# Performance work log

Hardware: AMD Instinct MI355X
Metric: run time of the kernel (lower is better)

The kernel has to match this reference:

```python
import jax, jax.numpy as jnp
import numpy as np

EPS = 1e-12
W_MAX = 0.8
ALPHA_MAX = 1.5
T = 10
ETA = 0.2
ALPHA_SCALE = 1.0
N = 50000
IN_DIM = 512
HID = 256
C = 8
EH = 64
E2 = 400000  # undirected pairs; E = 2*E2 directed edges


def setup_inputs() -> dict:
    key = jax.random.key(0)
    ks = jax.random.split(key, 12)
    x = jax.random.normal(ks[0], (N, IN_DIM), jnp.float32)
    src0 = jax.random.randint(ks[1], (E2,), 0, N)
    dst0 = jax.random.randint(ks[2], (E2,), 0, N)
    edge_index = jnp.concatenate([jnp.stack([src0, dst0]), jnp.stack([dst0, src0])], axis=1)
    rev = jnp.concatenate([jnp.arange(E2) + E2, jnp.arange(E2)])
    def lin(k, i, o):
        return jax.random.normal(k, (i, o), jnp.float32) * (2.0 / i) ** 0.5
    enc_w1 = lin(ks[3], IN_DIM, HID); enc_b1 = jnp.zeros((HID,), jnp.float32)
    enc_w2 = lin(ks[4], HID, C); enc_b2 = jnp.zeros((C,), jnp.float32)
    edge_w1 = lin(ks[5], 2 * HID + 2, EH); edge_b1 = jnp.zeros((EH,), jnp.float32)
    edge_w2 = lin(ks[6], EH, 1); edge_b2 = jnp.zeros((1,), jnp.float32)
    bound = (6.0 / (C + C)) ** 0.5  # xavier_uniform
    R_raw = jax.random.uniform(ks[7], (C, C), jnp.float32, -bound, bound) + 0.5 * jnp.eye(C, dtype=jnp.float32)
    R_scale_log = jnp.float32(0.0)
    msg_logit = jnp.float32(-3.0)
    return dict(x=x, edge_index=edge_index, rev=rev,
                enc_w1=enc_w1, enc_b1=enc_b1, enc_w2=enc_w2, enc_b2=enc_b2,
                edge_w1=edge_w1, edge_b1=edge_b1, edge_w2=edge_w2, edge_b2=edge_b2,
                R_raw=R_raw, R_scale_log=R_scale_log, msg_logit=msg_logit)


def reference(x, edge_index, rev, enc_w1, enc_b1, enc_w2, enc_b2,
              edge_w1, edge_b1, edge_w2, edge_b2, R_raw, R_scale_log, msg_logit):
    num_nodes = x.shape[0]
    src, dst = edge_index[0], edge_index[1]
    # unary encoder (mlp type, eval mode -> no dropout)
    h = jax.nn.relu(x @ enc_w1 + enc_b1)
    logits = h @ enc_w2 + enc_b2
    log_phi = jax.nn.log_softmax(logits, axis=-1)  # [N, C]
    # structural edge features from out-degree of src
    deg = jax.ops.segment_sum(jnp.ones_like(src, jnp.float32), src, num_segments=num_nodes)
    logdeg = jnp.log(deg + 1.0)
    a, b = logdeg[src], logdeg[dst]
    struct = jnp.stack([a + b, jnp.abs(a - b)], axis=-1)  # [E, 2]
    # learned symmetric edge weights -> per-edge kernel K
    hs, hd = h[src], h[dst]
    edge_in = jnp.concatenate([hs * hd, jnp.abs(hs - hd), struct], axis=-1)  # [E, 2H+2]
    eh = jax.nn.relu(edge_in @ edge_w1 + edge_b1)
    w_raw = (eh @ edge_w2 + edge_b2)[:, 0]
    w = W_MAX * jax.nn.sigmoid(w_raw)
    w = 0.5 * (w + w[rev])
    R = 0.5 * (R_raw + R_raw.T)
    R = (jax.nn.softplus(R_scale_log) + 1e-06) * jnp.tanh(R)
    K = jnp.exp(w[:, None, None] * R[None])  # [E, C, C]
    degc = jnp.maximum(deg, 1.0)
    edge_norm = (degc[src] * degc[dst]) ** -0.5  # [E]
    alpha = ALPHA_MAX * jax.nn.sigmoid(msg_logit) * ALPHA_SCALE
    lp_src = log_phi[src]
    m = jax.nn.softmax(lp_src, axis=-1)  # init_unary=True

    def step(m, _):
        f = jnp.einsum('ec,ecd->ed', m, K)
        log_f = jnp.log(jnp.maximum(f, EPS)) * edge_norm[:, None]
        sum_in = jax.ops.segment_sum(log_f, dst, num_segments=num_nodes)
        excl = sum_in[src] - log_f[rev]
        m_new = jax.nn.softmax(lp_src + alpha * excl, axis=-1)
        m = (1.0 - ETA) * m + ETA * m_new
        m = jnp.maximum(m, EPS)
        m = m / m.sum(axis=-1, keepdims=True)
        return m, None

    m, _ = jax.lax.scan(step, m, None, length=T)
    # beliefs
    f = jnp.einsum('ec,ecd->ed', m, K)
    log_f = jnp.log(jnp.maximum(f, EPS)) * edge_norm[:, None]
    sum_in = jax.ops.segment_sum(log_f, dst, num_segments=num_nodes)
    beliefs = jax.nn.softmax(log_phi + alpha * sum_in, axis=-1)
    return beliefs
```

## Files before the change

### kernel.cpp

```cpp
#include <hip/hip_runtime.h>
#include <cstddef>
#include <cstdint>

typedef _Float16 h4 __attribute__((ext_vector_type(4)));
typedef _Float16 h8 __attribute__((ext_vector_type(8)));
typedef float    f4 __attribute__((ext_vector_type(4)));
typedef int      i4 __attribute__((ext_vector_type(4)));

#define NN      50000
#define IND     512
#define HIDN    256
#define E2P     400000
#define EDD     800000
#define NBLK    196
#define SCN     50176
#define EBLK    1563
#define NBPN    1563

#define OFF_HF16    ((size_t)0)
#define OFF_LOGFA   ((size_t)0)
#define OFF_LOGFB   ((size_t)12800000)
#define OFF_Z       ((size_t)25600000)
#define OFF_DEG     ((size_t)28800000)
#define OFF_LOGDEG  ((size_t)29004800)
#define OFF_DEGC    ((size_t)29204800)
#define OFF_BASE    ((size_t)29404800)
#define OFF_CNT     ((size_t)29609600)
#define OFF_BLK     ((size_t)29814400)
#define OFF_WT      ((size_t)29818496)
#define OFF_BT      ((size_t)30080640)
#define OFF_RS      ((size_t)30150272)
#define OFF_WSYM    ((size_t)30150784)
#define OFF_POS     ((size_t)31750784)
#define OFF_ORDER   ((size_t)34950784)
#define OFF_BASE2   ((size_t)36550784)
#define OFF_OFS2    ((size_t)36755584)
#define OFF_EIS     ((size_t)36960384)
#define OFF_M       ((size_t)40160384)
#define OFF_WNS     ((size_t)52960384)
#define OFF_PPOS    ((size_t)59360384)
#define WS_NEED     ((size_t)62560384)

__device__ __forceinline__ int key2(int s, int d) {
    return ((s >> 10) << 10) | (d >> 6);
}

__device__ __forceinline__ int xcd_swz(int bid, int nwg) {
    int q = nwg >> 3, r = nwg & 7;
    int x = bid & 7, idx = bid >> 3;
    return (x < r ? x * (q + 1) : r * (q + 1) + (x - r) * q) + idx;
}

__global__ void k_deg(const int* __restrict__ ei, int* __restrict__ deg,
                      int* __restrict__ cnt2) {
    int e = blockIdx.x * 256 + threadIdx.x;
    int v = ei[e];
    atomicAdd(&deg[v], 1);
    if (e < E2P) {
        int d = ei[EDD + e];
        atomicAdd(&cnt2[key2(v, d)], 1);
    }
}

__global__ void k_node(const int* __restrict__ deg, float* __restrict__ logdeg,
                       float* __restrict__ degc) {
    int n = blockIdx.x * 256 + threadIdx.x;
    if (n < NN) {
        float d = (float)deg[n];
        logdeg[n] = logf(d + 1.0f);
        degc[n]   = fmaxf(d, 1.0f);
    }
}

__global__ void k_scan1(const int* __restrict__ deg, int* __restrict__ incl,
                        int* __restrict__ blk) {
    __shared__ int sm[256];
    int i = blockIdx.x * 256 + threadIdx.x;
    int v = deg[i];
    sm[threadIdx.x] = v;
    __syncthreads();
    for (int off = 1; off < 256; off <<= 1) {
        int t = (threadIdx.x >= off) ? sm[threadIdx.x - off] : 0;
        __syncthreads();
        sm[threadIdx.x] += t;
        __syncthreads();
    }
    incl[i] = sm[threadIdx.x];
    if (threadIdx.x == 255) blk[blockIdx.x] = sm[255];
}

__global__ void k_scan2(int* __restrict__ blk) {
    __shared__ int sm[256];
    int v = (threadIdx.x < NBLK) ? blk[threadIdx.x] : 0;
    sm[threadIdx.x] = v;
    __syncthreads();
    for (int off = 1; off < 256; off <<= 1) {
        int t = (threadIdx.x >= off) ? sm[threadIdx.x - off] : 0;
        __syncthreads();
        sm[threadIdx.x] += t;
        __syncthreads();
    }
    if (threadIdx.x < NBLK) blk[threadIdx.x] = sm[threadIdx.x];
}

__global__ void k_scan3(const int* __restrict__ incl, const int* __restrict__ deg,
                        const int* __restrict__ blk, int* __restrict__ base) {
    int i = blockIdx.x * 256 + threadIdx.x;
    int off = (blockIdx.x > 0) ? blk[blockIdx.x - 1] : 0;
    base[i] = off + incl[i] - deg[i];
}

__global__ void k_pos(const int* __restrict__ ei, const int* __restrict__ base,
                      int* __restrict__ cnt, int* __restrict__ pos) {
    int e = blockIdx.x * 256 + threadIdx.x;
    int dstn = ei[EDD + e];
    pos[e] = base[dstn] + atomicAdd(&cnt[dstn], 1);
}

__global__ void k_order(const int* __restrict__ ei, const int* __restrict__ base2,
                        int* __restrict__ ofs2, int* __restrict__ order) {
    int p = blockIdx.x * 256 + threadIdx.x;
    if (p < E2P) {
        int k = key2(ei[p], ei[EDD + p]);
        order[base2[k] + atomicAdd(&ofs2[k], 1)] = p;
    }
}

__global__ void k_gath(const int* __restrict__ ei, const int* __restrict__ order,
                       int2* __restrict__ eiS) {
    int i = blockIdx.x * 256 + threadIdx.x;
    if (i < E2P) {
        int p = order[i];
        eiS[i] = make_int2(ei[p], ei[EDD + p]);
    }
}

__global__ void k_prep(const float* __restrict__ enc_w1, const float* __restrict__ edge_w1,
                       const float* __restrict__ R_raw, const float* __restrict__ Rsl,
                       const float* __restrict__ mlog,
                       _Float16* __restrict__ Wt, _Float16* __restrict__ Bt,
                       float* __restrict__ Rs) {
    int gid = blockIdx.x * 256 + threadIdx.x;
    if (gid < 256 * 512) {
        int n = gid >> 9, k = gid & 511;
        Wt[n * 512 + k] = (_Float16)enc_w1[k * 256 + n];
        return;
    }
    int g2 = gid - 256 * 512;
    if (g2 < 64 * 544) {
        int n = g2 / 544, k = g2 - n * 544;
        float v = 0.0f;
        if (k < 512) {
            int tm = k >> 5, r = k & 31;
            int qq = r >> 3, jj = (r >> 1) & 3, typ = k & 1;
            int c = (tm >> 1) * 32 + qq * 8 + (tm & 1) * 4 + jj;
            v = edge_w1[(typ ? 256 + c : c) * 64 + n];
        } else if (k < 514) {
            v = edge_w1[k * 64 + n];
        }
        Bt[n * 544 + k] = (_Float16)v;
        return;
    }
    int g3 = g2 - 64 * 544;
    if (g3 < 64) {
        int c = g3 >> 3, d = g3 & 7;
        float rv = 0.5f * (R_raw[c * 8 + d] + R_raw[d * 8 + c]);
        float s  = log1pf(expf(Rsl[0])) + 1e-6f;
        Rs[g3] = s * tanhf(rv);
        return;
    }
    if (g3 == 64) {
        Rs[64] = 1.5f / (1.0f + expf(-mlog[0]));
    }
}

__global__ __launch_bounds__(256) void k_enc(const float* __restrict__ x,
                                             const _Float16* __restrict__ Wt,
                                             const float* __restrict__ b1,
                                             _Float16* __restrict__ hf) {
    __shared__ _Float16 WL[2][256 * 40];
    const int tid = threadIdx.x;
    const int wid = tid >> 6;
    const int lane = tid & 63;
    const int l15 = lane & 15;
    const int q = lane >> 4;
    const int m0 = blockIdx.x * 64;
    const int row = m0 + wid * 16 + l15;
    const bool ract = (row < NN);
    const float* xrow = x + (size_t)row * IND;

    f4 acc[16];
#pragma unroll
    for (int i = 0; i < 16; i++) acc[i] = (f4){0.f, 0.f, 0.f, 0.f};

    const int wn  = tid >> 2;
    const int wo  = (tid & 3) * 8;

    h8 wreg[4];
#pragma unroll
    for (int rep = 0; rep < 4; rep++)
        wreg[rep] = *(const h8*)(Wt + (size_t)(rep * 64 + wn) * IND + wo);
    f4 xa = (f4){0, 0, 0, 0}, xb = (f4){0, 0, 0, 0};
    if (ract) {
        const f4* xp = (const f4*)(xrow + q * 8);
        xa = xp[0]; xb = xp[1];
    }

    for (int kt = 0; kt < 16; kt++) {
        const int cur = kt & 1;
#pragma unroll
        for (int rep = 0; rep < 4; rep++)
            *(h8*)&WL[cur][(rep * 64 + wn) * 40 + wo] = wreg[rep];
        __syncthreads();
        f4 xa2, xb2;
        if (kt < 15) {
            const int kc = (kt + 1) * 32;
#pragma unroll
            for (int rep = 0; rep < 4; rep++)
                wreg[rep] = *(const h8*)(Wt + (size_t)(rep * 64 + wn) * IND + kc + wo);
            if (ract) {
                const f4* xp = (const f4*)(xrow + kc + q * 8);
                xa2 = xp[0]; xb2 = xp[1];
            }
        }
        h8 a;
#pragma unroll
        for (int u = 0; u < 4; u++) { a[u] = (_Float16)xa[u]; a[4 + u] = (_Float16)xb[u]; }
#pragma unroll
        for (int nt = 0; nt < 16; nt++) {
            h8 b = *(const h8*)&WL[cur][(nt * 16 + l15) * 40 + q * 8];
            acc[nt] = __builtin_amdgcn_mfma_f32_16x16x32_f16(a, b, acc[nt], 0, 0, 0);
        }
        if (kt < 15 && ract) { xa = xa2; xb = xb2; }
        __syncthreads();
    }
#pragma unroll
    for (int nt = 0; nt < 16; nt++) {
        int col = nt * 16 + l15;
        float bv = b1[col];
#pragma unroll
        for (int reg = 0; reg < 4; reg++) {
            int orow = m0 + wid * 16 + q * 4 + reg;
            if (orow < NN) {
                float v = acc[nt][reg] + bv;
                hf[(size_t)orow * HIDN + col] = (_Float16)fmaxf(v, 0.f);
            }
        }
    }
}

__global__ void k_logits(const _Float16* __restrict__ hf, const float* __restrict__ w2,
                         const float* __restrict__ b2, float* __restrict__ Z) {
    __shared__ float w2L[2048];
    for (int i = threadIdx.x; i < 2048; i += 256) w2L[i] = w2[i];
    __syncthreads();
    int n = blockIdx.x * 256 + threadIdx.x;
    if (n >= NN) return;
    float sum[8];
#pragma unroll
    for (int c = 0; c < 8; c++) sum[c] = b2[c];
    for (int kb = 0; kb < 32; kb++) {
        h8 hv = *(const h8*)(hf + (size_t)n * HIDN + kb * 8);
#pragma unroll
        for (int u = 0; u < 8; u++) {
            float hx = (float)hv[u];
            const float* wr = &w2L[(kb * 8 + u) * 8];
#pragma unroll
            for (int c = 0; c < 8; c++) sum[c] += hx * wr[c];
        }
    }
    float mx = sum[0];
#pragma unroll
    for (int c = 1; c < 8; c++) mx = fmaxf(mx, sum[c]);
    float se = 0.f;
#pragma unroll
    for (int c = 0; c < 8; c++) se += __expf(sum[c] - mx);
    float lse = __logf(se);
#pragma unroll
    for (int c = 0; c < 8; c++) Z[(size_t)n * 16 + c] = sum[c] - mx - lse;
}

__global__ __launch_bounds__(256) void k_edge(const int2* __restrict__ eiS,
        const _Float16* __restrict__ hf, const float* __restrict__ logdeg,
        const _Float16* __restrict__ BtG, const float* __restrict__ eb1,
        const float* __restrict__ ew2, const float* __restrict__ eb2,
        float* __restrict__ wsym2) {
    __shared__ _Float16 BtL[64 * 136];
    const int tid = threadIdx.x;
    const int wid = tid >> 6;
    const int lane = tid & 63;
    const int l15 = lane & 15;
    const int q = lane >> 4;
    const int eb = xcd_swz(blockIdx.x, gridDim.x) * 128;

    int sidx[2], didx[2];
    float la[2], lb[2];
#pragma unroll
    for (int mt = 0; mt < 2; mt++) {
        int e = eb + wid * 32 + mt * 16 + l15;
        int2 sd = eiS[e];
        sidx[mt] = sd.x;
        didx[mt] = sd.y;
        la[mt] = logdeg[sidx[mt]];
        lb[mt] = logdeg[didx[mt]];
    }

    f4 acc[2][4];
#pragma unroll
    for (int a = 0; a < 2; a++)
#pragma unroll
        for (int b = 0; b < 4; b++) acc[a][b] = (f4){0.f, 0.f, 0.f, 0.f};

    const _Float16* hq = hf + q * 8;
    h8 curS[2], curD[2];
#pragma unroll
    for (int mt = 0; mt < 2; mt++) {
        curS[mt] = *(const h8*)(hq + (size_t)sidx[mt] * HIDN);
        curD[mt] = *(const h8*)(hq + (size_t)didx[mt] * HIDN);
    }

    for (int ph = 0; ph < 4; ph++) {
        __syncthreads();
        {
            const int r = tid >> 2;
            const int c0 = tid & 3;
            const int kbase = ph * 128;
#pragma unroll
            for (int i2 = 0; i2 < 4; i2++) {
                int ck = c0 + i2 * 4;
                *(h8*)&BtL[r * 136 + ck * 8] =
                    *(const h8*)(BtG + (size_t)r * 544 + kbase + ck * 8);
            }
        }
        __syncthreads();
#pragma unroll
        for (int kk2 = 0; kk2 < 2; kk2++) {
            const int kk = ph * 2 + kk2;
            h8 nxtS[2], nxtD[2];
            if (kk < 7) {
                const int c1 = (kk + 1) * 32;
#pragma unroll
                for (int mt = 0; mt < 2; mt++) {
                    nxtS[mt] = *(const h8*)(hq + (size_t)sidx[mt] * HIDN + c1);
                    nxtD[mt] = *(const h8*)(hq + (size_t)didx[mt] * HIDN + c1);
                }
            }
            const int ko = kk2 * 64 + q * 8;
            {
                h8 a0[2];
#pragma unroll
                for (int mt = 0; mt < 2; mt++) {
#pragma unroll
                    for (int j = 0; j < 4; j++) {
                        float x1 = (float)curS[mt][j], x2 = (float)curD[mt][j];
                        a0[mt][2 * j]     = (_Float16)(x1 * x2);
                        a0[mt][2 * j + 1] = (_Float16)fabsf(x1 - x2);
                    }
                }
                h8 bf[4];
#pragma unroll
                for (int nt = 0; nt < 4; nt++)
                    bf[nt] = *(const h8*)&BtL[(nt * 16 + l15) * 136 + ko];
#pragma unroll
                for (int mt = 0; mt < 2; mt++)
#pragma unroll
                    for (int nt = 0; nt < 4; nt++)
                        acc[mt][nt] = __builtin_amdgcn_mfma_f32_16x16x32_f16(a0[mt], bf[nt], acc[mt][nt], 0, 0, 0);
            }
            {
                h8 a1[2];
#pragma unroll
                for (int mt = 0; mt < 2; mt++) {
#pragma unroll
                    for (int j = 0; j < 4; j++) {
                        float x1 = (float)curS[mt][4 + j], x2 = (float)curD[mt][4 + j];
                        a1[mt][2 * j]     = (_Float16)(x1 * x2);
                        a1[mt][2 * j + 1] = (_Float16)fabsf(x1 - x2);
                    }
                }
                h8 bf[4];
#pragma unroll
                for (int nt = 0; nt < 4; nt++)
                    bf[nt] = *(const h8*)&BtL[(nt * 16 + l15) * 136 + ko + 32];
#pragma unroll
                for (int mt = 0; mt < 2; mt++)
#pragma unroll
                    for (int nt = 0; nt < 4; nt++)
                        acc[mt][nt] = __builtin_amdgcn_mfma_f32_16x16x32_f16(a1[mt], bf[nt], acc[mt][nt], 0, 0, 0);
            }
            if (kk < 7) {
#pragma unroll
                for (int mt = 0; mt < 2; mt++) { curS[mt] = nxtS[mt]; curD[mt] = nxtD[mt]; }
            }
        }
    }

    __syncthreads();
    {
        const int r = tid >> 2, ck = tid & 3;
        *(h8*)&BtL[r * 136 + ck * 8] = *(const h8*)(BtG + (size_t)r * 544 + 512 + ck * 8);
    }
    __syncthreads();
    {
        h8 bf[4];
#pragma unroll
        for (int nt = 0; nt < 4; nt++)
            bf[nt] = *(const h8*)&BtL[(nt * 16 + l15) * 136 + q * 8];
#pragma unroll
        for (int mt = 0; mt < 2; mt++) {
            h8 a = (h8){0, 0, 0, 0, 0, 0, 0, 0};
            if (q == 0) {
                a[0] = (_Float16)(la[mt] + lb[mt]);
                a[1] = (_Float16)fabsf(la[mt] - lb[mt]);
            }
#pragma unroll
            for (int nt = 0; nt < 4; nt++)
                acc[mt][nt] = __builtin_amdgcn_mfma_f32_16x16x32_f16(a, bf[nt], acc[mt][nt], 0, 0, 0);
        }
    }

    float b1v[4], w2v[4];
#pragma unroll
    for (int nt = 0; nt < 4; nt++) {
        int col = nt * 16 + l15;
        b1v[nt] = eb1[col];
        w2v[nt] = ew2[col];
    }
    const float b2s = eb2[0];
    float part[2][4];
#pragma unroll
    for (int mt = 0; mt < 2; mt++)
#pragma unroll
        for (int reg = 0; reg < 4; reg++) {
            float s = 0.f;
#pragma unroll
            for (int nt = 0; nt < 4; nt++) {
                float v = acc[mt][nt][reg] + b1v[nt];
                s += fmaxf(v, 0.f) * w2v[nt];
            }
            part[mt][reg] = s;
        }
#pragma unroll
    for (int off = 1; off < 16; off <<= 1)
#pragma unroll
        for (int mt = 0; mt < 2; mt++)
#pragma unroll
            for (int reg = 0; reg < 4; reg++)
                part[mt][reg] += __shfl_xor(part[mt][reg], off, 64);
    if (l15 == 0) {
#pragma unroll
        for (int mt = 0; mt < 2; mt++)
#pragma unroll
            for (int reg = 0; reg < 4; reg++) {
                int er = eb + wid * 32 + mt * 16 + q * 4 + reg;
                if (er < E2P) {
                    float xr = part[mt][reg] + b2s;
                    wsym2[er] = 0.8f / (1.0f + __expf(-xr));
                }
            }
    }
}


__device__ __forceinline__ void kprod1(const float* __restrict__ RsL, float w,
                                       const float* m, float* f) {
#pragma unroll
    for (int d = 0; d < 8; d++) f[d] = 0.f;
#pragma unroll
    for (int c = 0; c < 8; c++) {
        {
            float kv = __expf(w * RsL[c * 8 + c]);
            f[c] += m[c] * kv;
        }
#pragma unroll
        for (int d = c + 1; d < 8; d++) {
            float kv = __expf(w * RsL[c * 8 + d]);
            f[d] += m[c] * kv;
            f[c] += m[d] * kv;
        }
    }
}

__global__ __launch_bounds__(256) void k_init(const int2* __restrict__ eiS,
        const float* __restrict__ wsym2, const float* __restrict__ degc,
        const float* __restrict__ Rs, const float* __restrict__ Z,
        const int* __restrict__ pos, const int* __restrict__ order,
        float2* __restrict__ wnS, int* __restrict__ ppos,
        _Float16* __restrict__ M, _Float16* __restrict__ logfA) {
    __shared__ float RsL[64];
    const int tid = threadIdx.x;
    if (tid < 64) RsL[tid] = Rs[tid];
    __syncthreads();
    int i = xcd_swz(blockIdx.x, EBLK) * 256 + tid;
    if (i >= E2P) return;
    int p = order[i];
    int2 sd = eiS[i];
    int sp = sd.x, dp = sd.y;
    float w = wsym2[i];
    float nrm = rsqrtf(degc[sp] * degc[dp]);
    int pz0 = pos[p];
    int pz1 = pos[E2P + p];
    wnS[pz0] = make_float2(w, nrm);
    wnS[pz1] = make_float2(w, nrm);
    ppos[pz0] = pz1;
    ppos[pz1] = pz0;
    const f4* Zs = (const f4*)(Z + (size_t)sp * 16);
    const f4* Zd = (const f4*)(Z + (size_t)dp * 16);
    f4 ls0 = Zs[0], ls1 = Zs[1], ld0 = Zd[0], ld1 = Zd[1];
    float lps[8], lpd[8];
#pragma unroll
    for (int u = 0; u < 4; u++) { lps[u] = ls0[u]; lps[4+u] = ls1[u]; lpd[u] = ld0[u]; lpd[4+u] = ld1[u]; }
    float me[8], mr[8];
    {
        float mx = lps[0], mx2 = lpd[0];
#pragma unroll
        for (int d = 1; d < 8; d++) { mx = fmaxf(mx, lps[d]); mx2 = fmaxf(mx2, lpd[d]); }
        float s = 0.f, s2 = 0.f;
#pragma unroll
        for (int d = 0; d < 8; d++) { me[d] = __expf(lps[d] - mx); s += me[d];
                                      mr[d] = __expf(lpd[d] - mx2); s2 += mr[d]; }
        float rs = 1.f / s, rs2 = 1.f / s2;
#pragma unroll
        for (int d = 0; d < 8; d++) { me[d] *= rs; mr[d] *= rs2; }
    }
    {
        h8 mh, mh2;
#pragma unroll
        for (int d = 0; d < 8; d++) { mh[d] = (_Float16)me[d]; mh2[d] = (_Float16)mr[d]; }
        *(h8*)(M + (size_t)pz1 * 8) = mh;
        *(h8*)(M + (size_t)pz0 * 8) = mh2;
    }
    float fe[8], fr[8];
    kprod1(RsL, w, me, fe);
    kprod1(RsL, w, mr, fr);
    h8 le, lr;
#pragma unroll
    for (int d = 0; d < 8; d++) {
        le[d] = (_Float16)(__logf(fmaxf(fe[d], 1e-12f)) * nrm);
        lr[d] = (_Float16)(__logf(fmaxf(fr[d], 1e-12f)) * nrm);
    }
    *(h8*)(logfA + (size_t)pz0 * 8) = le;
    *(h8*)(logfA + (size_t)pz1 * 8) = lr;
}

__global__ __launch_bounds__(256) void k_bpN(const float* __restrict__ Rs,
        const float* __restrict__ Z, const int* __restrict__ base,
        const int* __restrict__ deg, const float2* __restrict__ wnS,
        const int* __restrict__ ppos, _Float16* __restrict__ M,
        const _Float16* __restrict__ lfA, _Float16* __restrict__ lfB) {
    __shared__ float RsL[64];
    const int tid = threadIdx.x;
    if (tid < 64) RsL[tid] = Rs[tid];
    __syncthreads();
    int g = xcd_swz(blockIdx.x, NBPN) * 256 + tid;
    int n = g >> 3;
    if (n >= NN) return;
    const int j = tid & 7;
    const int b = base[n], cnt = deg[n];
    const float alpha = Rs[64];
    const f4* Zr = (const f4*)(Z + (size_t)n * 16);
    f4 z0 = Zr[0], z1 = Zr[1];
    float lp[8];
#pragma unroll
    for (int u = 0; u < 4; u++) { lp[u] = z0[u]; lp[4 + u] = z1[u]; }
    float S[8];
#pragma unroll
    for (int d = 0; d < 8; d++) S[d] = 0.f;
    for (int s = j; s < cnt; s += 8) {
        h8 v = *(const h8*)(lfA + (size_t)(b + s) * 8);
#pragma unroll
        for (int d = 0; d < 8; d++) S[d] += (float)v[d];
    }
#pragma unroll
    for (int off = 1; off < 8; off <<= 1)
#pragma unroll
        for (int d = 0; d < 8; d++) S[d] += __shfl_xor(S[d], off, 64);
    for (int s = j; s < cnt; s += 8) {
        const int sl = b + s;
        h8 lfh = *(const h8*)(lfA + (size_t)sl * 8);
        h8 mh  = *(const h8*)(M + (size_t)sl * 8);
        float2 wn = wnS[sl];
        float t[8], m1[8];
#pragma unroll
        for (int d = 0; d < 8; d++)
            t[d] = lp[d] + alpha * (S[d] - (float)lfh[d]);
        float mx = t[0];
#pragma unroll
        for (int d = 1; d < 8; d++) mx = fmaxf(mx, t[d]);
        float ssum = 0.f;
#pragma unroll
        for (int d = 0; d < 8; d++) { m1[d] = __expf(t[d] - mx); ssum += m1[d]; }
        float rs = 1.f / ssum, t1 = 0.f;
#pragma unroll
        for (int d = 0; d < 8; d++) {
            m1[d] = fmaxf(0.8f * (float)mh[d] + 0.2f * m1[d] * rs, 1e-12f);
            t1 += m1[d];
        }
        float rt = 1.f / t1;
#pragma unroll
        for (int d = 0; d < 8; d++) m1[d] *= rt;
        h8 mo;
#pragma unroll
        for (int d = 0; d < 8; d++) mo[d] = (_Float16)m1[d];
        *(h8*)(M + (size_t)sl * 8) = mo;
        float f2[8];
        kprod1(RsL, wn.x, m1, f2);
        h8 le;
#pragma unroll
        for (int d = 0; d < 8; d++)
            le[d] = (_Float16)(__logf(fmaxf(f2[d], 1e-12f)) * wn.y);
        *(h8*)(lfB + (size_t)ppos[sl] * 8) = le;
    }
}

__global__ void k_sum(const _Float16* __restrict__ logf, const int* __restrict__ base,
                      const int* __restrict__ deg, const float* __restrict__ Z,
                      const float* __restrict__ Rs, float* __restrict__ out) {
    int g = blockIdx.x * 256 + threadIdx.x;
    int n = g >> 3;
    if (n >= NN) return;
    int j = threadIdx.x & 7;
    int b = base[n], cnt = deg[n];
    float acc[8];
#pragma unroll
    for (int d = 0; d < 8; d++) acc[d] = 0.f;
    for (int s = j; s < cnt; s += 8) {
        h8 v = *(const h8*)(logf + (size_t)(b + s) * 8);
#pragma unroll
        for (int d = 0; d < 8; d++) acc[d] += (float)v[d];
    }
    int lane = threadIdx.x & 63;
    float v4[4], v2[2], r;
    {
        bool hi = (lane & 4) != 0;
#pragma unroll
        for (int i = 0; i < 4; i++) {
            float send = hi ? acc[i] : acc[i + 4];
            float recv = __shfl_xor(send, 4, 64);
            v4[i] = (hi ? acc[i + 4] : acc[i]) + recv;
        }
    }
    {
        bool hi = (lane & 2) != 0;
#pragma unroll
        for (int i = 0; i < 2; i++) {
            float send = hi ? v4[i] : v4[i + 2];
            float recv = __shfl_xor(send, 2, 64);
            v2[i] = (hi ? v4[i + 2] : v4[i]) + recv;
        }
    }
    {
        bool hi = (lane & 1) != 0;
        float send = hi ? v2[0] : v2[1];
        float recv = __shfl_xor(send, 1, 64);
        r = (hi ? v2[1] : v2[0]) + recv;
    }
    float alpha = Rs[64];
    float v = Z[(size_t)n * 16 + j] + alpha * r;
    float mx = v;
    mx = fmaxf(mx, __shfl_xor(mx, 1, 64));
    mx = fmaxf(mx, __shfl_xor(mx, 2, 64));
    mx = fmaxf(mx, __shfl_xor(mx, 4, 64));
    float ex = __expf(v - mx);
    float s = ex;
    s += __shfl_xor(s, 1, 64); s += __shfl_xor(s, 2, 64); s += __shfl_xor(s, 4, 64);
    out[(size_t)n * 8 + j] = ex / s;
}

extern "C" void kernel_launch(void* const* d_in, const int* in_sizes, int n_in,
                              void* d_out, int out_size, void* d_ws, size_t ws_size,
                              hipStream_t stream) {
    if (ws_size < WS_NEED) return;
    const float* x        = (const float*)d_in[0];
    const int*   ei       = (const int*)d_in[1];
    const float* enc_w1   = (const float*)d_in[3];
    const float* enc_b1   = (const float*)d_in[4];
    const float* enc_w2   = (const float*)d_in[5];
    const float* enc_b2   = (const float*)d_in[6];
    const float* edge_w1  = (const float*)d_in[7];
    const float* edge_b1  = (const float*)d_in[8];
    const float* edge_w2  = (const float*)d_in[9];
    const float* edge_b2  = (const float*)d_in[10];
    const float* R_raw    = (const float*)d_in[11];
    const float* Rsl      = (const float*)d_in[12];
    const float* mlog     = (const float*)d_in[13];

    char* ws = (char*)d_ws;
    _Float16* hf     = (_Float16*)(ws + OFF_HF16);
    _Float16* lfA    = (_Float16*)(ws + OFF_LOGFA);
    _Float16* lfB    = (_Float16*)(ws + OFF_LOGFB);
    float* Zb        = (float*)(ws + OFF_Z);
    int*   deg       = (int*)  (ws + OFF_DEG);
    float* logdeg    = (float*)(ws + OFF_LOGDEG);
    float* degc      = (float*)(ws + OFF_DEGC);
    int*   baseA     = (int*)  (ws + OFF_BASE);
    int*   cnt       = (int*)  (ws + OFF_CNT);
    int*   blk       = (int*)  (ws + OFF_BLK);
    _Float16* Wt     = (_Float16*)(ws + OFF_WT);
    _Float16* Bt     = (_Float16*)(ws + OFF_BT);
    float* Rs        = (float*)(ws + OFF_RS);
    float* wsym2     = (float*)(ws + OFF_WSYM);
    int*   pos       = (int*)  (ws + OFF_POS);
    int*   order     = (int*)  (ws + OFF_ORDER);
    int*   base2     = (int*)  (ws + OFF_BASE2);
    int*   ofs2      = (int*)  (ws + OFF_OFS2);
    int2*  eiS       = (int2*) (ws + OFF_EIS);
    _Float16* Mb     = (_Float16*)(ws + OFF_M);
    float2* wnS      = (float2*)(ws + OFF_WNS);
    int*   ppos      = (int*)  (ws + OFF_PPOS);
    float* outp      = (float*)d_out;

    hipMemsetAsync(deg, 0, (size_t)SCN * 4, stream);
    hipMemsetAsync(ofs2, 0, (size_t)SCN * 4, stream);
    k_deg<<<dim3(EDD / 256), dim3(256), 0, stream>>>(ei, deg, ofs2);
    k_node<<<dim3(NBLK), dim3(256), 0, stream>>>(deg, logdeg, degc);
    k_prep<<<dim3((256 * 512 + 64 * 544 + 65 + 255) / 256), dim3(256), 0, stream>>>(
        enc_w1, edge_w1, R_raw, Rsl, mlog, Wt, Bt, Rs);
    k_scan1<<<dim3(NBLK), dim3(256), 0, stream>>>(deg, cnt , blk);
    k_scan2<<<dim3(1), dim3(256), 0, stream>>>(blk);
    k_scan3<<<dim3(NBLK), dim3(256), 0, stream>>>(cnt, deg, blk, baseA);
    hipMemsetAsync(cnt, 0, (size_t)SCN * 4, stream);
    k_pos<<<dim3(EDD / 256), dim3(256), 0, stream>>>(ei, baseA, cnt, pos);
    k_scan1<<<dim3(NBLK), dim3(256), 0, stream>>>(ofs2, cnt, blk);
    k_scan2<<<dim3(1), dim3(256), 0, stream>>>(blk);
    k_scan3<<<dim3(NBLK), dim3(256), 0, stream>>>(cnt, ofs2, blk, base2);
    hipMemsetAsync(ofs2, 0, (size_t)SCN * 4, stream);
    k_order<<<dim3(EBLK), dim3(256), 0, stream>>>(ei, base2, ofs2, order);
    k_gath<<<dim3(EBLK), dim3(256), 0, stream>>>(ei, order, eiS);
    k_enc<<<dim3((NN + 63) / 64), dim3(256), 0, stream>>>(x, Wt, enc_b1, hf);
    k_logits<<<dim3(NBLK), dim3(256), 0, stream>>>(hf, enc_w2, enc_b2, Zb);
    k_edge<<<dim3(E2P / 128), dim3(256), 0, stream>>>(eiS, hf, logdeg, Bt, edge_b1,
                                                      edge_w2, edge_b2, wsym2);
    k_init<<<dim3(EBLK), dim3(256), 0, stream>>>(eiS, wsym2, degc, Rs, Zb, pos, order,
                                                 wnS, ppos, Mb, lfA);
    _Float16* cur = lfA;
    _Float16* nxt = lfB;
    for (int t = 0; t < 10; t++) {
        k_bpN<<<dim3(NBPN), dim3(256), 0, stream>>>(Rs, Zb, baseA, deg, wnS, ppos,
                                                    Mb, cur, nxt);
        _Float16* tmp = cur; cur = nxt; nxt = tmp;
    }
    k_sum<<<dim3((NN * 8 + 255) / 256), dim3(256), 0, stream>>>(cur, baseA, deg, Zb,
                                                                Rs, outp);
    (void)in_sizes; (void)n_in; (void)out_size;
}
```

Measured before the change: 805.0 us.

## Switch BP log-message storage to source-ordered layout with LDS-staged block gather

The BP step now writes log-messages contiguously at the edge's own slot and gathers incoming ones through ppos. Each block handles 32 nodes and stages their gathered log-messages in LDS, so the segment sums and the per-edge updates reuse them instead of rereading global memory. Scattered writes become coalesced writes, and the random access moves to the read side. The encoder GEMM also preloads the whole x row strip into registers and fully unrolls its K loop, which raises register pressure (launch bounds set to one block).

```diff
diff --git a/kernel.cpp b/kernel.cpp
--- a/kernel.cpp
+++ b/kernel.cpp
@@ -16,6 +16,7 @@
 #define SCN     50176
 #define EBLK    1563
 #define NBPN    1563
+#define BCAP    1024
 
 #define OFF_HF16    ((size_t)0)
 #define OFF_LOGFA   ((size_t)0)
@@ -174,10 +175,10 @@
     }
 }
 
-__global__ __launch_bounds__(256) void k_enc(const float* __restrict__ x,
-                                             const _Float16* __restrict__ Wt,
-                                             const float* __restrict__ b1,
-                                             _Float16* __restrict__ hf) {
+__global__ __launch_bounds__(256, 1) void k_enc(const float* __restrict__ x,
+                                                const _Float16* __restrict__ Wt,
+                                                const float* __restrict__ b1,
+                                                _Float16* __restrict__ hf) {
     __shared__ _Float16 WL[2][256 * 40];
     const int tid = threadIdx.x;
     const int wid = tid >> 6;
@@ -189,49 +190,56 @@
     const bool ract = (row < NN);
     const float* xrow = x + (size_t)row * IND;
 
+    f4 xk0[16], xk1[16];
+#pragma unroll
+    for (int kt = 0; kt < 16; kt++) {
+        if (ract) {
+            const f4* xp = (const f4*)(xrow + kt * 32 + q * 8);
+            xk0[kt] = xp[0]; xk1[kt] = xp[1];
+        } else {
+            xk0[kt] = (f4){0, 0, 0, 0}; xk1[kt] = (f4){0, 0, 0, 0};
+        }
+    }
+    h8 xh[16];
+#pragma unroll
+    for (int kt = 0; kt < 16; kt++) {
+#pragma unroll
+        for (int u = 0; u < 4; u++) {
+            xh[kt][u]     = (_Float16)xk0[kt][u];
+            xh[kt][4 + u] = (_Float16)xk1[kt][u];
+        }
+    }
+
     f4 acc[16];
 #pragma unroll
     for (int i = 0; i < 16; i++) acc[i] = (f4){0.f, 0.f, 0.f, 0.f};
 
-    const int wn  = tid >> 2;
-    const int wo  = (tid & 3) * 8;
+    const int wn = tid >> 2;
+    const int wo = (tid & 3) * 8;
 
     h8 wreg[4];
 #pragma unroll
     for (int rep = 0; rep < 4; rep++)
         wreg[rep] = *(const h8*)(Wt + (size_t)(rep * 64 + wn) * IND + wo);
-    f4 xa = (f4){0, 0, 0, 0}, xb = (f4){0, 0, 0, 0};
-    if (ract) {
-        const f4* xp = (const f4*)(xrow + q * 8);
-        xa = xp[0]; xb = xp[1];
-    }
-
+
+#pragma unroll
     for (int kt = 0; kt < 16; kt++) {
         const int cur = kt & 1;
 #pragma unroll
         for (int rep = 0; rep < 4; rep++)
             *(h8*)&WL[cur][(rep * 64 + wn) * 40 + wo] = wreg[rep];
         __syncthreads();
-        f4 xa2, xb2;
         if (kt < 15) {
             const int kc = (kt + 1) * 32;
 #pragma unroll
             for (int rep = 0; rep < 4; rep++)
                 wreg[rep] = *(const h8*)(Wt + (size_t)(rep * 64 + wn) * IND + kc + wo);
-            if (ract) {
-                const f4* xp = (const f4*)(xrow + kc + q * 8);
-                xa2 = xp[0]; xb2 = xp[1];
-            }
-        }
-        h8 a;
-#pragma unroll
-        for (int u = 0; u < 4; u++) { a[u] = (_Float16)xa[u]; a[4 + u] = (_Float16)xb[u]; }
+        }
 #pragma unroll
         for (int nt = 0; nt < 16; nt++) {
             h8 b = *(const h8*)&WL[cur][(nt * 16 + l15) * 40 + q * 8];
-            acc[nt] = __builtin_amdgcn_mfma_f32_16x16x32_f16(a, b, acc[nt], 0, 0, 0);
-        }
-        if (kt < 15 && ract) { xa = xa2; xb = xb2; }
+            acc[nt] = __builtin_amdgcn_mfma_f32_16x16x32_f16(xh[kt], b, acc[nt], 0, 0, 0);
+        }
         __syncthreads();
     }
 #pragma unroll
@@ -539,51 +547,82 @@
         le[d] = (_Float16)(__logf(fmaxf(fe[d], 1e-12f)) * nrm);
         lr[d] = (_Float16)(__logf(fmaxf(fr[d], 1e-12f)) * nrm);
     }
-    *(h8*)(logfA + (size_t)pz0 * 8) = le;
-    *(h8*)(logfA + (size_t)pz1 * 8) = lr;
+    *(h8*)(logfA + (size_t)pz1 * 8) = le;
+    *(h8*)(logfA + (size_t)pz0 * 8) = lr;
 }
 
 __global__ __launch_bounds__(256) void k_bpN(const float* __restrict__ Rs,
         const float* __restrict__ Z, const int* __restrict__ base,
-        const int* __restrict__ deg, const float2* __restrict__ wnS,
-        const int* __restrict__ ppos, _Float16* __restrict__ M,
-        const _Float16* __restrict__ lfA, _Float16* __restrict__ lfB) {
+        const float2* __restrict__ wnS, const int* __restrict__ ppos,
+        _Float16* __restrict__ M, const _Float16* __restrict__ lfP,
+        _Float16* __restrict__ lfO) {
     __shared__ float RsL[64];
+    __shared__ int   segs[33];
+    __shared__ float ZL[32][8];
+    __shared__ float SL[32][8];
+    __shared__ _Float16 lfL[BCAP][8];
+    __shared__ unsigned char nlL[BCAP];
     const int tid = threadIdx.x;
+    const int n0 = xcd_swz(blockIdx.x, gridDim.x) * 32;
     if (tid < 64) RsL[tid] = Rs[tid];
-    __syncthreads();
-    int g = xcd_swz(blockIdx.x, NBPN) * 256 + tid;
-    int n = g >> 3;
-    if (n >= NN) return;
-    const int j = tid & 7;
-    const int b = base[n], cnt = deg[n];
+    if (tid < 33) segs[tid] = base[n0 + tid];
+    if (tid >= 64 && tid < 96) {
+        int nl = tid - 64;
+        if (n0 + nl < NN) {
+            const f4* zp = (const f4*)(Z + (size_t)(n0 + nl) * 16);
+            f4 a = zp[0], b2 = zp[1];
+#pragma unroll
+            for (int u = 0; u < 4; u++) { ZL[nl][u] = a[u]; ZL[nl][4 + u] = b2[u]; }
+        }
+    }
+    __syncthreads();
+    const int s0 = segs[0];
+    const int count = segs[32] - s0;
     const float alpha = Rs[64];
-    const f4* Zr = (const f4*)(Z + (size_t)n * 16);
-    f4 z0 = Zr[0], z1 = Zr[1];
-    float lp[8];
-#pragma unroll
-    for (int u = 0; u < 4; u++) { lp[u] = z0[u]; lp[4 + u] = z1[u]; }
-    float S[8];
-#pragma unroll
-    for (int d = 0; d < 8; d++) S[d] = 0.f;
-    for (int s = j; s < cnt; s += 8) {
-        h8 v = *(const h8*)(lfA + (size_t)(b + s) * 8);
-#pragma unroll
-        for (int d = 0; d < 8; d++) S[d] += (float)v[d];
-    }
-#pragma unroll
-    for (int off = 1; off < 8; off <<= 1)
-#pragma unroll
-        for (int d = 0; d < 8; d++) S[d] += __shfl_xor(S[d], off, 64);
-    for (int s = j; s < cnt; s += 8) {
-        const int sl = b + s;
-        h8 lfh = *(const h8*)(lfA + (size_t)sl * 8);
-        h8 mh  = *(const h8*)(M + (size_t)sl * 8);
+    for (int k = tid; k < count; k += 256) {
+        int pp = ppos[s0 + k];
+        h8 v = *(const h8*)(lfP + (size_t)pp * 8);
+        if (k < BCAP) *(h8*)&lfL[k][0] = v;
+    }
+    __syncthreads();
+    {
+        const int nl = tid >> 3, j = tid & 7;
+        const int sb = segs[nl] - s0;
+        const int cnt = segs[nl + 1] - segs[nl];
+        float S[8];
+#pragma unroll
+        for (int d = 0; d < 8; d++) S[d] = 0.f;
+        for (int s = j; s < cnt; s += 8) {
+            int k = sb + s;
+            h8 v;
+            if (k < BCAP) { v = *(h8*)&lfL[k][0]; nlL[k] = (unsigned char)nl; }
+            else          { v = *(const h8*)(lfP + (size_t)ppos[s0 + k] * 8); }
+#pragma unroll
+            for (int d = 0; d < 8; d++) S[d] += (float)v[d];
+        }
+#pragma unroll
+        for (int off = 1; off < 8; off <<= 1)
+#pragma unroll
+            for (int d = 0; d < 8; d++) S[d] += __shfl_xor(S[d], off, 64);
+        SL[nl][j] = S[j];
+    }
+    __syncthreads();
+    for (int k = tid; k < count; k += 256) {
+        const int sl = s0 + k;
+        int nl;
+        h8 lfh;
+        if (k < BCAP) { nl = nlL[k]; lfh = *(h8*)&lfL[k][0]; }
+        else {
+            nl = 0;
+            for (int a2 = 1; a2 < 32; a2++) if (segs[a2] <= sl) nl = a2;
+            lfh = *(const h8*)(lfP + (size_t)ppos[sl] * 8);
+        }
+        h8 mh = *(const h8*)(M + (size_t)sl * 8);
         float2 wn = wnS[sl];
         float t[8], m1[8];
 #pragma unroll
         for (int d = 0; d < 8; d++)
-            t[d] = lp[d] + alpha * (S[d] - (float)lfh[d]);
+            t[d] = ZL[nl][d] + alpha * (SL[nl][d] - (float)lfh[d]);
         float mx = t[0];
 #pragma unroll
         for (int d = 1; d < 8; d++) mx = fmaxf(mx, t[d]);
@@ -609,13 +648,14 @@
 #pragma unroll
         for (int d = 0; d < 8; d++)
             le[d] = (_Float16)(__logf(fmaxf(f2[d], 1e-12f)) * wn.y);
-        *(h8*)(lfB + (size_t)ppos[sl] * 8) = le;
+        *(h8*)(lfO + (size_t)sl * 8) = le;
     }
 }
 
 __global__ void k_sum(const _Float16* __restrict__ logf, const int* __restrict__ base,
-                      const int* __restrict__ deg, const float* __restrict__ Z,
-                      const float* __restrict__ Rs, float* __restrict__ out) {
+                      const int* __restrict__ deg, const int* __restrict__ ppos,
+                      const float* __restrict__ Z, const float* __restrict__ Rs,
+                      float* __restrict__ out) {
     int g = blockIdx.x * 256 + threadIdx.x;
     int n = g >> 3;
     if (n >= NN) return;
@@ -625,7 +665,7 @@
 #pragma unroll
     for (int d = 0; d < 8; d++) acc[d] = 0.f;
     for (int s = j; s < cnt; s += 8) {
-        h8 v = *(const h8*)(logf + (size_t)(b + s) * 8);
+        h8 v = *(const h8*)(logf + (size_t)ppos[b + s] * 8);
 #pragma unroll
         for (int d = 0; d < 8; d++) acc[d] += (float)v[d];
     }
@@ -736,11 +776,11 @@
     _Float16* cur = lfA;
     _Float16* nxt = lfB;
     for (int t = 0; t < 10; t++) {
-        k_bpN<<<dim3(NBPN), dim3(256), 0, stream>>>(Rs, Zb, baseA, deg, wnS, ppos,
+        k_bpN<<<dim3(NBPN), dim3(256), 0, stream>>>(Rs, Zb, baseA, wnS, ppos,
                                                     Mb, cur, nxt);
         _Float16* tmp = cur; cur = nxt; nxt = tmp;
     }
-    k_sum<<<dim3((NN * 8 + 255) / 256), dim3(256), 0, stream>>>(cur, baseA, deg, Zb,
-                                                                Rs, outp);
+    k_sum<<<dim3((NN * 8 + 255) / 256), dim3(256), 0, stream>>>(cur, baseA, deg, ppos,
+                                                                Zb, Rs, outp);
     (void)in_sizes; (void)n_in; (void)out_size;
 }
```

Result: slower. 835.7 us (+3.8%).
